# Kernel tuning notes

Hardware: AMD Instinct MI355X
Metric: run time of the kernel (lower is better)

## Reference

```python
import jax, jax.numpy as jnp
import numpy as np

N = 100000       # num nodes
E = 1000000      # num edges
D_IN = 128       # node_input_dim
H = 128          # hidden_dim
D_E = 32         # edge_input_dim
C = 16           # num_classes


def setup_inputs() -> dict:
    key = jax.random.key(0)
    ks = jax.random.split(key, 8)
    x = jax.random.normal(ks[0], (N, D_IN), dtype=jnp.float32)
    edge_index = jax.random.randint(ks[1], (2, E), 0, N)
    edge_attr = jax.random.normal(ks[2], (E, D_E), dtype=jnp.float32)

    def glorot(k, shape):
        fan = shape[0]
        return (jax.random.normal(k, shape, dtype=jnp.float32) / np.sqrt(fan)).astype(jnp.float32)

    W1 = glorot(ks[3], (D_IN, H)); b1 = jnp.zeros((H,), jnp.float32)
    W2 = glorot(ks[4], (H, H));    b2 = jnp.zeros((H,), jnp.float32)
    W3 = glorot(ks[5], (H, H));    b3 = jnp.zeros((H,), jnp.float32)
    W_fc = glorot(ks[6], (D_E + 2 * H, C)); b_fc = jnp.zeros((C,), jnp.float32)
    return {"x": x, "edge_index": edge_index, "edge_attr": edge_attr,
            "W1": W1, "b1": b1, "W2": W2, "b2": b2, "W3": W3, "b3": b3,
            "W_fc": W_fc, "b_fc": b_fc}


def gcn_conv(h_in, W, b, src, dst, dinv):
    """PyG GCNConv: h = D^-1/2 (A+I) D^-1/2 (h_in @ W) + b.
    Self-loop contribution handled analytically as dinv[i]^2 * h[i]."""
    h = h_in @ W                                      # [N, H]
    norm = dinv[src] * dinv[dst]                      # [E]
    msgs = h[src] * norm[:, None]                     # gather + scale, [E, H]
    agg = jax.ops.segment_sum(msgs, dst, num_segments=N)  # scatter-add
    agg = agg + h * (dinv * dinv)[:, None]            # self-loops
    return agg + b


def reference(x, edge_index, edge_attr, W1, b1, W2, b2, W3, b3, W_fc, b_fc):
    src, dst = edge_index[0], edge_index[1]
    # degree with self-loops (edge_weight = 1), as in PyG gcn_norm
    deg = jax.ops.segment_sum(jnp.ones((E,), jnp.float32), dst, num_segments=N) + 1.0
    dinv = jax.lax.rsqrt(deg)

    h = jax.nn.relu(gcn_conv(x, W1, b1, src, dst, dinv))
    # dropout(p=0.3) is identity in eval mode
    h = jax.nn.relu(gcn_conv(h, W2, b2, src, dst, dinv))
    h = jax.nn.relu(gcn_conv(h, W3, b3, src, dst, dinv))

    edge_features = jnp.concatenate([h[src], h[dst], edge_attr], axis=1)  # [E, 2H+D_E]
    edge_output = edge_features @ W_fc + b_fc                             # [E, C]
    return jax.nn.log_softmax(edge_output, axis=1)
```

## Files before the change

kernel.cpp:

```cpp
#include <hip/hip_runtime.h>
#include <hip/hip_bf16.h>

#define D_IN 128
#define HDIM 128
#define D_E  32
#define NC   16
#define SCAN_CHUNK 2048

typedef __attribute__((ext_vector_type(8))) short short8;
typedef __attribute__((ext_vector_type(4))) float float4v;

__device__ inline short f2bs(float f) {
  __hip_bfloat16 h = (__hip_bfloat16)f;
  return *reinterpret_cast<short*>(&h);
}

__device__ inline float bs2f(short s) {
  unsigned int u = ((unsigned int)(unsigned short)s) << 16;
  float f;
  __builtin_memcpy(&f, &u, 4);
  return f;
}


__global__ __launch_bounds__(256) void count_deg(const int* __restrict__ ei, int* __restrict__ deg, int E) {
  int e = blockIdx.x * 256 + threadIdx.x;
  if (e < E) atomicAdd(&deg[ei[E + e]], 1);
}

__global__ __launch_bounds__(256) void scan_blocksums(const int* __restrict__ deg, int* __restrict__ bsum, int n) {
  __shared__ int red[256];
  int t = threadIdx.x;
  int base = blockIdx.x * SCAN_CHUNK + t * 8;
  int s = 0;
#pragma unroll
  for (int j = 0; j < 8; ++j) {
    int i = base + j;
    if (i < n) s += deg[i];
  }
  red[t] = s;
  __syncthreads();
  for (int off = 128; off > 0; off >>= 1) {
    if (t < off) red[t] += red[t + off];
    __syncthreads();
  }
  if (t == 0) bsum[blockIdx.x] = red[0];
}

__global__ __launch_bounds__(256) void scan_offsets(const int* __restrict__ bsum, int* __restrict__ boff, int nb) {
  __shared__ int s[256];
  int t = threadIdx.x;
  int v = (t < nb) ? bsum[t] : 0;
  s[t] = v;
  __syncthreads();
  for (int off = 1; off < 256; off <<= 1) {
    int u = (t >= off) ? s[t - off] : 0;
    __syncthreads();
    s[t] += u;
    __syncthreads();
  }
  if (t < nb) boff[t] = (t == 0) ? 0 : s[t - 1];
}

__global__ __launch_bounds__(256) void scan_write(const int* __restrict__ deg, const int* __restrict__ boff,
                                                  int* __restrict__ rowptr, float* __restrict__ dinv, int n) {
  __shared__ int red[256];
  int t = threadIdx.x;
  int base = blockIdx.x * SCAN_CHUNK + t * 8;
  int v[8];
  int s = 0;
#pragma unroll
  for (int j = 0; j < 8; ++j) {
    int i = base + j;
    v[j] = (i < n) ? deg[i] : 0;
    s += v[j];
  }
  red[t] = s;
  __syncthreads();
  for (int off = 1; off < 256; off <<= 1) {
    int u = (t >= off) ? red[t - off] : 0;
    __syncthreads();
    red[t] += u;
    __syncthreads();
  }
  int run = red[t] - s + boff[blockIdx.x];
#pragma unroll
  for (int j = 0; j < 8; ++j) {
    int i = base + j;
    if (i < n) {
      rowptr[i] = run;
      dinv[i] = rsqrtf((float)v[j] + 1.0f);
    }
    run += v[j];
  }
}

__global__ __launch_bounds__(256) void fill_csr(const int* __restrict__ ei, const int* __restrict__ rowptr,
                                                int* __restrict__ cursor, int* __restrict__ col, int E) {
  int e = blockIdx.x * 256 + threadIdx.x;
  if (e < E) {
    int d = ei[E + e];
    int pos = atomicAdd(&cursor[d], 1);
    col[rowptr[d] + pos] = ei[e];
  }
}

__global__ __launch_bounds__(256) void repack_w128(const float* __restrict__ W, short* __restrict__ wp) {
  int idx = blockIdx.x * 256 + threadIdx.x;
  if (idx < 16384) {
    int j = idx & 7, lane = (idx >> 3) & 63, t = (idx >> 9) & 7, kc = idx >> 12;
    int k = kc * 32 + (lane >> 4) * 8 + j;
    int nn = t * 16 + (lane & 15);
    wp[idx] = f2bs(W[k * HDIM + nn]);
  }
}

__global__ __launch_bounds__(256) void repack_wcp(const float* __restrict__ Wfc, short* __restrict__ wp) {
  int idx = blockIdx.x * 256 + threadIdx.x;
  if (idx < 4096) {
    int j = idx & 7, lane = (idx >> 3) & 63, t = (idx >> 9) & 1, kc = idx >> 10;
    int k = kc * 32 + (lane >> 4) * 8 + j;
    int nn = t * 16 + (lane & 15);
    float v = (nn < 16) ? Wfc[k * NC + nn] : Wfc[(HDIM + k) * NC + (nn - 16)];
    wp[idx] = f2bs(v);
  }
}

__global__ __launch_bounds__(256) void repack_wea(const float* __restrict__ Wfc, short* __restrict__ wp) {
  int idx = blockIdx.x * 256 + threadIdx.x;
  if (idx < 512) {
    int j = idx & 7, lane = (idx >> 3) & 63;
    int k = (lane >> 4) * 8 + j;
    int nn = lane & 15;
    wp[idx] = f2bs(Wfc[(2 * HDIM + k) * NC + nn]);
  }
}

template<int NCOL, bool FP32IN, bool FP32OUT, bool SCALE>
__global__ __launch_bounds__(256) void gemm_mfma(const void* __restrict__ Xv, const short* __restrict__ wpack,
                                                 void* __restrict__ Yv, const float* __restrict__ dscale, int n) {
  constexpr int NT = NCOL / 16;
  __shared__ short sw[4 * NT * 512];
  int tid = threadIdx.x;
  {
    const float4* wg = (const float4*)wpack;
    float4* sg = (float4*)sw;
    for (int i = tid; i < 4 * NT * 512 / 8; i += 256) sg[i] = wg[i];
  }
  __syncthreads();
  int wave = tid >> 6, lane = tid & 63;
  int quad = lane >> 4;
  int row = blockIdx.x * 64 + wave * 16 + (lane & 15);
  bool rowok = row < n;
  float4v acc[NT];
#pragma unroll
  for (int t = 0; t < NT; ++t) acc[t] = (float4v){0.f, 0.f, 0.f, 0.f};

#pragma unroll
  for (int kc = 0; kc < 4; ++kc) {
    short8 af = {0, 0, 0, 0, 0, 0, 0, 0};
    if (rowok) {
      if (FP32IN) {
        const float* xp = (const float*)Xv + (size_t)row * 128 + kc * 32 + quad * 8;
        float4 x0 = *(const float4*)xp;
        float4 x1 = *(const float4*)(xp + 4);
        af[0] = f2bs(x0.x); af[1] = f2bs(x0.y); af[2] = f2bs(x0.z); af[3] = f2bs(x0.w);
        af[4] = f2bs(x1.x); af[5] = f2bs(x1.y); af[6] = f2bs(x1.z); af[7] = f2bs(x1.w);
      } else {
        af = *(const short8*)((const short*)Xv + (size_t)row * 128 + kc * 32 + quad * 8);
      }
    }
#pragma unroll
    for (int t = 0; t < NT; ++t) {
      short8 bfr = *(const short8*)(sw + (kc * NT + t) * 512 + lane * 8);
      acc[t] = __builtin_amdgcn_mfma_f32_16x16x32_bf16(af, bfr, acc[t], 0, 0, 0);
    }
  }
  int orow0 = blockIdx.x * 64 + wave * 16 + quad * 4;
  float dv[4] = {1.f, 1.f, 1.f, 1.f};
  if constexpr (SCALE) {
#pragma unroll
    for (int r = 0; r < 4; ++r) dv[r] = (orow0 + r < n) ? dscale[orow0 + r] : 0.f;
  }
#pragma unroll
  for (int t = 0; t < NT; ++t) {
    int ocol = t * 16 + (lane & 15);
#pragma unroll
    for (int r = 0; r < 4; ++r) {
      int orow = orow0 + r;
      if (orow < n) {
        float val = acc[t][r];
        if constexpr (SCALE) val *= dv[r];
        if (FP32OUT)
          ((float*)Yv)[(size_t)orow * NCOL + ocol] = val;
        else
          ((__hip_bfloat16*)Yv)[(size_t)orow * NCOL + ocol] = (__hip_bfloat16)val;
      }
    }
  }
}

__global__ __launch_bounds__(256) void gemm_ea(const float* __restrict__ ea, const short* __restrict__ wp,
                                               const float* __restrict__ bfc, __hip_bfloat16* __restrict__ EA, int E) {
  __shared__ short sw[512];
  __shared__ float sb[16];
  int tid = threadIdx.x;
  if (tid < 64) ((float4*)sw)[tid] = ((const float4*)wp)[tid];
  if (tid < 16) sb[tid] = bfc[tid];
  __syncthreads();
  int wave = tid >> 6, lane = tid & 63, quad = lane >> 4;
  int row = blockIdx.x * 64 + wave * 16 + (lane & 15);
  short8 af = {0, 0, 0, 0, 0, 0, 0, 0};
  if (row < E) {
    const float* xp = ea + (size_t)row * D_E + quad * 8;
    float4 x0 = *(const float4*)xp;
    float4 x1 = *(const float4*)(xp + 4);
    af[0] = f2bs(x0.x); af[1] = f2bs(x0.y); af[2] = f2bs(x0.z); af[3] = f2bs(x0.w);
    af[4] = f2bs(x1.x); af[5] = f2bs(x1.y); af[6] = f2bs(x1.z); af[7] = f2bs(x1.w);
  }
  short8 bfr = *(const short8*)(sw + lane * 8);
  float4v acc = (float4v){0.f, 0.f, 0.f, 0.f};
  acc = __builtin_amdgcn_mfma_f32_16x16x32_bf16(af, bfr, acc, 0, 0, 0);
  int orow0 = blockIdx.x * 64 + wave * 16 + quad * 4;
  int ocol = lane & 15;
  float bb = sb[ocol];
#pragma unroll
  for (int r = 0; r < 4; ++r) {
    int orow = orow0 + r;
    if (orow < E) EA[(size_t)orow * NC + ocol] = (__hip_bfloat16)(acc[r] + bb);
  }
}

__global__ __launch_bounds__(256) void agg_vec(const __hip_bfloat16* __restrict__ hs, const float* __restrict__ dinv,
                                               const int* __restrict__ rowptr, const int* __restrict__ deg,
                                               const int* __restrict__ col, const float* __restrict__ bias,
                                               __hip_bfloat16* __restrict__ hout, int N) {
  int tid = threadIdx.x;
  int wave = tid >> 6, lane = tid & 63;
  int q = lane >> 4, ft = lane & 15;
  int i = blockIdx.x * 16 + wave * 4 + q;
  bool ok = i < N;
  int iS = ok ? i : (N - 1);
  int s0 = rowptr[iS];
  int dg = ok ? deg[iS] : 0;
  float di = dinv[iS];
  const short* hb = (const short*)hs;
  short8 selfv = *(const short8*)(hb + (size_t)iS * 128 + ft * 8);
  float acc[8];
#pragma unroll
  for (int j = 0; j < 8; ++j) acc[j] = bs2f(selfv[j]);
  int mx = dg;
  mx = max(mx, __shfl_xor(mx, 16));
  mx = max(mx, __shfl_xor(mx, 32));
  int cA = 0, cB = 0, cC = 0, cD = 0;
  if (0 < dg) cA = col[s0];
  if (1 < dg) cB = col[s0 + 1];
  if (2 < dg) cC = col[s0 + 2];
  if (3 < dg) cD = col[s0 + 3];
  for (int it = 0; it < mx; it += 4) {
    int nA = 0, nB = 0, nC = 0, nD = 0;
    if (it + 4 < dg) nA = col[s0 + it + 4];
    if (it + 5 < dg) nB = col[s0 + it + 5];
    if (it + 6 < dg) nC = col[s0 + it + 6];
    if (it + 7 < dg) nD = col[s0 + it + 7];
    if (it < dg) {
      short8 r0 = *(const short8*)(hb + (size_t)cA * 128 + ft * 8);
#pragma unroll
      for (int j = 0; j < 8; ++j) acc[j] += bs2f(r0[j]);
    }
    if (it + 1 < dg) {
      short8 r1 = *(const short8*)(hb + (size_t)cB * 128 + ft * 8);
#pragma unroll
      for (int j = 0; j < 8; ++j) acc[j] += bs2f(r1[j]);
    }
    if (it + 2 < dg) {
      short8 r2 = *(const short8*)(hb + (size_t)cC * 128 + ft * 8);
#pragma unroll
      for (int j = 0; j < 8; ++j) acc[j] += bs2f(r2[j]);
    }
    if (it + 3 < dg) {
      short8 r3 = *(const short8*)(hb + (size_t)cD * 128 + ft * 8);
#pragma unroll
      for (int j = 0; j < 8; ++j) acc[j] += bs2f(r3[j]);
    }
    cA = nA; cB = nB; cC = nC; cD = nD;
  }
  if (ok) {
    float4 b0 = *(const float4*)(bias + ft * 8);
    float4 b1 = *(const float4*)(bias + ft * 8 + 4);
    float bb[8] = {b0.x, b0.y, b0.z, b0.w, b1.x, b1.y, b1.z, b1.w};
    short8 o;
#pragma unroll
    for (int j = 0; j < 8; ++j) {
      float v = fmaxf(fmaf(acc[j], di, bb[j]), 0.f);
      o[j] = f2bs(v);
    }
    *(short8*)((short*)hout + (size_t)i * 128 + ft * 8) = o;
  }
}

__global__ __launch_bounds__(256) void edge_final(const int* __restrict__ ei, const __hip_bfloat16* __restrict__ EA,
                                                  const float* __restrict__ PQ, float* __restrict__ out, int E) {
  int e = blockIdx.x * 256 + threadIdx.x;
  bool ok = e < E;
  int ec = ok ? e : (E - 1);
  int s = ei[ec], d = ei[E + ec];
  const float4* p1 = (const float4*)(PQ + (size_t)s * 32);
  const float4* p2 = (const float4*)(PQ + (size_t)d * 32 + 16);
  const short* eb = (const short*)EA + (size_t)ec * NC;
  short8 ev0 = *(const short8*)eb;
  short8 ev1 = *(const short8*)(eb + 8);
  float l[NC];
  float4 P0 = p1[0], P1 = p1[1], P2 = p1[2], P3 = p1[3];
  float4 Q0 = p2[0], Q1 = p2[1], Q2 = p2[2], Q3 = p2[3];
  l[0]  = P0.x + Q0.x + bs2f(ev0[0]);
  l[1]  = P0.y + Q0.y + bs2f(ev0[1]);
  l[2]  = P0.z + Q0.z + bs2f(ev0[2]);
  l[3]  = P0.w + Q0.w + bs2f(ev0[3]);
  l[4]  = P1.x + Q1.x + bs2f(ev0[4]);
  l[5]  = P1.y + Q1.y + bs2f(ev0[5]);
  l[6]  = P1.z + Q1.z + bs2f(ev0[6]);
  l[7]  = P1.w + Q1.w + bs2f(ev0[7]);
  l[8]  = P2.x + Q2.x + bs2f(ev1[0]);
  l[9]  = P2.y + Q2.y + bs2f(ev1[1]);
  l[10] = P2.z + Q2.z + bs2f(ev1[2]);
  l[11] = P2.w + Q2.w + bs2f(ev1[3]);
  l[12] = P3.x + Q3.x + bs2f(ev1[4]);
  l[13] = P3.y + Q3.y + bs2f(ev1[5]);
  l[14] = P3.z + Q3.z + bs2f(ev1[6]);
  l[15] = P3.w + Q3.w + bs2f(ev1[7]);
  float m = l[0];
#pragma unroll
  for (int c = 1; c < NC; ++c) m = fmaxf(m, l[c]);
  float sum = 0.f;
#pragma unroll
  for (int c = 0; c < NC; ++c) sum += __expf(l[c] - m);
  float lse = __logf(sum) + m;
  if (ok) {
    float4* po = (float4*)(out + (size_t)e * NC);
    po[0] = make_float4(l[0] - lse, l[1] - lse, l[2] - lse, l[3] - lse);
    po[1] = make_float4(l[4] - lse, l[5] - lse, l[6] - lse, l[7] - lse);
    po[2] = make_float4(l[8] - lse, l[9] - lse, l[10] - lse, l[11] - lse);
    po[3] = make_float4(l[12] - lse, l[13] - lse, l[14] - lse, l[15] - lse);
  }
}


extern "C" void kernel_launch(void* const* d_in, const int* in_sizes, int n_in,
                              void* d_out, int out_size, void* d_ws, size_t ws_size,
                              hipStream_t stream) {
  const float* x   = (const float*)d_in[0];
  const int*   ei  = (const int*)d_in[1];
  const float* ea  = (const float*)d_in[2];
  const float* W1  = (const float*)d_in[3];
  const float* b1  = (const float*)d_in[4];
  const float* W2  = (const float*)d_in[5];
  const float* b2  = (const float*)d_in[6];
  const float* W3  = (const float*)d_in[7];
  const float* b3  = (const float*)d_in[8];
  const float* Wfc = (const float*)d_in[9];
  const float* bfc = (const float*)d_in[10];
  float* out = (float*)d_out;
  int N = in_sizes[0] / D_IN;
  int E = in_sizes[1] / 2;

  char* w = (char*)d_ws;
  size_t off = 0;
  auto alloc = [&](size_t bytes) -> char* {
    char* p = w + off;
    off += (bytes + 255) & ~(size_t)255;
    return p;
  };
  __hip_bfloat16* A = (__hip_bfloat16*)alloc((size_t)N * HDIM * 2);
  __hip_bfloat16* B = (__hip_bfloat16*)alloc((size_t)N * HDIM * 2);
  float* PQ     = (float*)alloc((size_t)N * 32 * 4);
  __hip_bfloat16* EA = (__hip_bfloat16*)alloc((size_t)E * NC * 2);
  int*   col    = (int*)alloc((size_t)E * 4);
  int*   deg    = (int*)alloc((size_t)N * 4);
  int*   cursor = (int*)alloc((size_t)N * 4);
  float* dinv   = (float*)alloc((size_t)N * 4);
  int*   rowptr = (int*)alloc((size_t)N * 4);
  int*   bsum   = (int*)alloc(1024 * 4);
  int*   boff   = (int*)alloc(1024 * 4);
  short* wp1    = (short*)alloc(16384 * 2);
  short* wp2    = (short*)alloc(16384 * 2);
  short* wp3    = (short*)alloc(16384 * 2);
  short* wpc    = (short*)alloc(4096 * 2);
  short* wpe    = (short*)alloc(512 * 2);

  hipMemsetAsync(deg, 0, (size_t)N * 4, stream);
  hipMemsetAsync(cursor, 0, (size_t)N * 4, stream);

  int eb = (E + 255) / 256;
  int sb = (N + SCAN_CHUNK - 1) / SCAN_CHUNK;
  count_deg<<<eb, 256, 0, stream>>>(ei, deg, E);
  scan_blocksums<<<sb, 256, 0, stream>>>(deg, bsum, N);
  scan_offsets<<<1, 256, 0, stream>>>(bsum, boff, sb);
  scan_write<<<sb, 256, 0, stream>>>(deg, boff, rowptr, dinv, N);
  fill_csr<<<eb, 256, 0, stream>>>(ei, rowptr, cursor, col, E);
  repack_w128<<<64, 256, 0, stream>>>(W1, wp1);
  repack_w128<<<64, 256, 0, stream>>>(W2, wp2);
  repack_w128<<<64, 256, 0, stream>>>(W3, wp3);
  repack_wcp<<<16, 256, 0, stream>>>(Wfc, wpc);
  repack_wea<<<2, 256, 0, stream>>>(Wfc, wpe);

  int gb = (N + 63) / 64;
  int ab = (N + 15) / 16;
  int geb = (E + 63) / 64;
  gemm_ea<<<geb, 256, 0, stream>>>(ea, wpe, bfc, EA, E);
  gemm_mfma<128, true,  false, true ><<<gb, 256, 0, stream>>>(x, wp1, A, dinv, N);
  agg_vec<<<ab, 256, 0, stream>>>(A, dinv, rowptr, deg, col, b1, B, N);
  gemm_mfma<128, false, false, true ><<<gb, 256, 0, stream>>>(B, wp2, A, dinv, N);
  agg_vec<<<ab, 256, 0, stream>>>(A, dinv, rowptr, deg, col, b2, B, N);
  gemm_mfma<128, false, false, true ><<<gb, 256, 0, stream>>>(B, wp3, A, dinv, N);
  agg_vec<<<ab, 256, 0, stream>>>(A, dinv, rowptr, deg, col, b3, B, N);
  gemm_mfma<32,  false, true,  false><<<gb, 256, 0, stream>>>(B, wpc, PQ, nullptr, N);
  edge_final<<<eb, 256, 0, stream>>>(ei, EA, PQ, out, E);
}
```

Before: 620.4 us.

## Fuse edge-attr GEMM into edge softmax kernel and cooperatively load CSR indices

Folds the edge_attr projection MFMA into the final edge kernel. This removes the intermediate EA buffer write and read, plus one launch. The log-softmax now uses 16-lane shuffles, with each lane owning one class. The aggregation kernel now loads 16 neighbor indices per quad in one coalesced read and broadcasts them with shuffles, replacing the per-lane prefetch of 4. The costs are scalar, less-coalesced output stores and PQ gathers in the fused kernel, and more shuffle work.

```diff
diff --git a/kernel.cpp b/kernel.cpp
--- a/kernel.cpp
+++ b/kernel.cpp
@@ -197,37 +197,6 @@
           ((__hip_bfloat16*)Yv)[(size_t)orow * NCOL + ocol] = (__hip_bfloat16)val;
       }
     }
-  }
-}
-
-__global__ __launch_bounds__(256) void gemm_ea(const float* __restrict__ ea, const short* __restrict__ wp,
-                                               const float* __restrict__ bfc, __hip_bfloat16* __restrict__ EA, int E) {
-  __shared__ short sw[512];
-  __shared__ float sb[16];
-  int tid = threadIdx.x;
-  if (tid < 64) ((float4*)sw)[tid] = ((const float4*)wp)[tid];
-  if (tid < 16) sb[tid] = bfc[tid];
-  __syncthreads();
-  int wave = tid >> 6, lane = tid & 63, quad = lane >> 4;
-  int row = blockIdx.x * 64 + wave * 16 + (lane & 15);
-  short8 af = {0, 0, 0, 0, 0, 0, 0, 0};
-  if (row < E) {
-    const float* xp = ea + (size_t)row * D_E + quad * 8;
-    float4 x0 = *(const float4*)xp;
-    float4 x1 = *(const float4*)(xp + 4);
-    af[0] = f2bs(x0.x); af[1] = f2bs(x0.y); af[2] = f2bs(x0.z); af[3] = f2bs(x0.w);
-    af[4] = f2bs(x1.x); af[5] = f2bs(x1.y); af[6] = f2bs(x1.z); af[7] = f2bs(x1.w);
-  }
-  short8 bfr = *(const short8*)(sw + lane * 8);
-  float4v acc = (float4v){0.f, 0.f, 0.f, 0.f};
-  acc = __builtin_amdgcn_mfma_f32_16x16x32_bf16(af, bfr, acc, 0, 0, 0);
-  int orow0 = blockIdx.x * 64 + wave * 16 + quad * 4;
-  int ocol = lane & 15;
-  float bb = sb[ocol];
-#pragma unroll
-  for (int r = 0; r < 4; ++r) {
-    int orow = orow0 + r;
-    if (orow < E) EA[(size_t)orow * NC + ocol] = (__hip_bfloat16)(acc[r] + bb);
   }
 }
 
@@ -249,41 +218,18 @@
   float acc[8];
 #pragma unroll
   for (int j = 0; j < 8; ++j) acc[j] = bs2f(selfv[j]);
-  int mx = dg;
-  mx = max(mx, __shfl_xor(mx, 16));
-  mx = max(mx, __shfl_xor(mx, 32));
-  int cA = 0, cB = 0, cC = 0, cD = 0;
-  if (0 < dg) cA = col[s0];
-  if (1 < dg) cB = col[s0 + 1];
-  if (2 < dg) cC = col[s0 + 2];
-  if (3 < dg) cD = col[s0 + 3];
-  for (int it = 0; it < mx; it += 4) {
-    int nA = 0, nB = 0, nC = 0, nD = 0;
-    if (it + 4 < dg) nA = col[s0 + it + 4];
-    if (it + 5 < dg) nB = col[s0 + it + 5];
-    if (it + 6 < dg) nC = col[s0 + it + 6];
-    if (it + 7 < dg) nD = col[s0 + it + 7];
-    if (it < dg) {
-      short8 r0 = *(const short8*)(hb + (size_t)cA * 128 + ft * 8);
-#pragma unroll
-      for (int j = 0; j < 8; ++j) acc[j] += bs2f(r0[j]);
-    }
-    if (it + 1 < dg) {
-      short8 r1 = *(const short8*)(hb + (size_t)cB * 128 + ft * 8);
-#pragma unroll
-      for (int j = 0; j < 8; ++j) acc[j] += bs2f(r1[j]);
-    }
-    if (it + 2 < dg) {
-      short8 r2 = *(const short8*)(hb + (size_t)cC * 128 + ft * 8);
-#pragma unroll
-      for (int j = 0; j < 8; ++j) acc[j] += bs2f(r2[j]);
-    }
-    if (it + 3 < dg) {
-      short8 r3 = *(const short8*)(hb + (size_t)cD * 128 + ft * 8);
-#pragma unroll
-      for (int j = 0; j < 8; ++j) acc[j] += bs2f(r3[j]);
-    }
-    cA = nA; cB = nB; cC = nC; cD = nD;
+  for (int b = 0; b < dg; b += 16) {
+    int rem = dg - b;
+    int myidx = (ft < rem) ? col[s0 + b + ft] : 0;
+#pragma unroll
+    for (int k = 0; k < 16; ++k) {
+      if (k < rem) {
+        int ck = __shfl(myidx, (q << 4) + k);
+        short8 r = *(const short8*)(hb + (size_t)ck * 128 + ft * 8);
+#pragma unroll
+        for (int j = 0; j < 8; ++j) acc[j] += bs2f(r[j]);
+      }
+    }
   }
   if (ok) {
     float4 b0 = *(const float4*)(bias + ft * 8);
@@ -299,49 +245,53 @@
   }
 }
 
-__global__ __launch_bounds__(256) void edge_final(const int* __restrict__ ei, const __hip_bfloat16* __restrict__ EA,
+__global__ __launch_bounds__(256) void edge_fused(const int* __restrict__ ei, const float* __restrict__ ea,
+                                                  const short* __restrict__ wpe, const float* __restrict__ bfc,
                                                   const float* __restrict__ PQ, float* __restrict__ out, int E) {
-  int e = blockIdx.x * 256 + threadIdx.x;
-  bool ok = e < E;
-  int ec = ok ? e : (E - 1);
-  int s = ei[ec], d = ei[E + ec];
-  const float4* p1 = (const float4*)(PQ + (size_t)s * 32);
-  const float4* p2 = (const float4*)(PQ + (size_t)d * 32 + 16);
-  const short* eb = (const short*)EA + (size_t)ec * NC;
-  short8 ev0 = *(const short8*)eb;
-  short8 ev1 = *(const short8*)(eb + 8);
-  float l[NC];
-  float4 P0 = p1[0], P1 = p1[1], P2 = p1[2], P3 = p1[3];
-  float4 Q0 = p2[0], Q1 = p2[1], Q2 = p2[2], Q3 = p2[3];
-  l[0]  = P0.x + Q0.x + bs2f(ev0[0]);
-  l[1]  = P0.y + Q0.y + bs2f(ev0[1]);
-  l[2]  = P0.z + Q0.z + bs2f(ev0[2]);
-  l[3]  = P0.w + Q0.w + bs2f(ev0[3]);
-  l[4]  = P1.x + Q1.x + bs2f(ev0[4]);
-  l[5]  = P1.y + Q1.y + bs2f(ev0[5]);
-  l[6]  = P1.z + Q1.z + bs2f(ev0[6]);
-  l[7]  = P1.w + Q1.w + bs2f(ev0[7]);
-  l[8]  = P2.x + Q2.x + bs2f(ev1[0]);
-  l[9]  = P2.y + Q2.y + bs2f(ev1[1]);
-  l[10] = P2.z + Q2.z + bs2f(ev1[2]);
-  l[11] = P2.w + Q2.w + bs2f(ev1[3]);
-  l[12] = P3.x + Q3.x + bs2f(ev1[4]);
-  l[13] = P3.y + Q3.y + bs2f(ev1[5]);
-  l[14] = P3.z + Q3.z + bs2f(ev1[6]);
-  l[15] = P3.w + Q3.w + bs2f(ev1[7]);
-  float m = l[0];
-#pragma unroll
-  for (int c = 1; c < NC; ++c) m = fmaxf(m, l[c]);
-  float sum = 0.f;
-#pragma unroll
-  for (int c = 0; c < NC; ++c) sum += __expf(l[c] - m);
-  float lse = __logf(sum) + m;
-  if (ok) {
-    float4* po = (float4*)(out + (size_t)e * NC);
-    po[0] = make_float4(l[0] - lse, l[1] - lse, l[2] - lse, l[3] - lse);
-    po[1] = make_float4(l[4] - lse, l[5] - lse, l[6] - lse, l[7] - lse);
-    po[2] = make_float4(l[8] - lse, l[9] - lse, l[10] - lse, l[11] - lse);
-    po[3] = make_float4(l[12] - lse, l[13] - lse, l[14] - lse, l[15] - lse);
+  __shared__ short sw[512];
+  __shared__ float sb[16];
+  int tid = threadIdx.x;
+  if (tid < 64) ((float4*)sw)[tid] = ((const float4*)wpe)[tid];
+  if (tid < 16) sb[tid] = bfc[tid];
+  __syncthreads();
+  int wave = tid >> 6, lane = tid & 63, quad = lane >> 4;
+  int row = blockIdx.x * 64 + wave * 16 + (lane & 15);
+  short8 af = {0, 0, 0, 0, 0, 0, 0, 0};
+  if (row < E) {
+    const float* xp = ea + (size_t)row * D_E + quad * 8;
+    float4 x0 = *(const float4*)xp;
+    float4 x1 = *(const float4*)(xp + 4);
+    af[0] = f2bs(x0.x); af[1] = f2bs(x0.y); af[2] = f2bs(x0.z); af[3] = f2bs(x0.w);
+    af[4] = f2bs(x1.x); af[5] = f2bs(x1.y); af[6] = f2bs(x1.z); af[7] = f2bs(x1.w);
+  }
+  short8 bfr = *(const short8*)(sw + lane * 8);
+  float4v acc = (float4v){0.f, 0.f, 0.f, 0.f};
+  acc = __builtin_amdgcn_mfma_f32_16x16x32_bf16(af, bfr, acc, 0, 0, 0);
+  int c = lane & 15;
+  int orow0 = blockIdx.x * 64 + wave * 16 + quad * 4;
+  float bb = sb[c];
+  float ps[4], pd[4];
+#pragma unroll
+  for (int r = 0; r < 4; ++r) {
+    int orow = orow0 + r;
+    int er = (orow < E) ? orow : (E - 1);
+    int s = ei[er], d = ei[E + er];
+    ps[r] = PQ[(size_t)s * 32 + c];
+    pd[r] = PQ[(size_t)d * 32 + 16 + c];
+  }
+#pragma unroll
+  for (int r = 0; r < 4; ++r) {
+    float l = acc[r] + bb + ps[r] + pd[r];
+    float m = l;
+#pragma unroll
+    for (int w = 1; w < 16; w <<= 1) m = fmaxf(m, __shfl_xor(m, w));
+    float ex = __expf(l - m);
+    float sum = ex;
+#pragma unroll
+    for (int w = 1; w < 16; w <<= 1) sum += __shfl_xor(sum, w);
+    float lse = __logf(sum) + m;
+    int orow = orow0 + r;
+    if (orow < E) out[(size_t)orow * NC + c] = l - lse;
   }
 }
 
@@ -374,7 +324,6 @@
   __hip_bfloat16* A = (__hip_bfloat16*)alloc((size_t)N * HDIM * 2);
   __hip_bfloat16* B = (__hip_bfloat16*)alloc((size_t)N * HDIM * 2);
   float* PQ     = (float*)alloc((size_t)N * 32 * 4);
-  __hip_bfloat16* EA = (__hip_bfloat16*)alloc((size_t)E * NC * 2);
   int*   col    = (int*)alloc((size_t)E * 4);
   int*   deg    = (int*)alloc((size_t)N * 4);
   int*   cursor = (int*)alloc((size_t)N * 4);
@@ -407,7 +356,6 @@
   int gb = (N + 63) / 64;
   int ab = (N + 15) / 16;
   int geb = (E + 63) / 64;
-  gemm_ea<<<geb, 256, 0, stream>>>(ea, wpe, bfc, EA, E);
   gemm_mfma<128, true,  false, true ><<<gb, 256, 0, stream>>>(x, wp1, A, dinv, N);
   agg_vec<<<ab, 256, 0, stream>>>(A, dinv, rowptr, deg, col, b1, B, N);
   gemm_mfma<128, false, false, true ><<<gb, 256, 0, stream>>>(B, wp2, A, dinv, N);
@@ -415,5 +363,5 @@
   gemm_mfma<128, false, false, true ><<<gb, 256, 0, stream>>>(B, wp3, A, dinv, N);
   agg_vec<<<ab, 256, 0, stream>>>(A, dinv, rowptr, deg, col, b3, B, N);
   gemm_mfma<32,  false, true,  false><<<gb, 256, 0, stream>>>(B, wpc, PQ, nullptr, N);
-  edge_final<<<eb, 256, 0, stream>>>(ei, EA, PQ, out, E);
-}
+  edge_fused<<<geb, 256, 0, stream>>>(ei, ea, wpe, bfc, PQ, out, E);
+}
```

After: 581.4 us. 6.3% less time.
